# Kernel tuning notes

Hardware: AMD Instinct MI355X
Metric: run time of the kernel (lower is better)

## Reference

```python
import jax, jax.numpy as jnp
import numpy as np

N = 100000      # nodes
E = 3200000     # edges (before self-loops)
F_IN = 512      # input feature dim
HEADS = 8
DIM = 8         # per-head dim for hidden layers
HID = HEADS * DIM  # 64
CLS = 40        # num_classes
NEG_SLOPE = 0.2 # PyG GATConv default leaky relu slope


def setup_inputs() -> dict:
    key = jax.random.key(0)
    ks = jax.random.split(key, 14)
    def glorot(k, shape, fan_in):
        return jax.random.normal(k, shape, jnp.float32) * (1.0 / np.sqrt(fan_in))
    return {
        "x": jax.random.normal(ks[0], (N, F_IN), jnp.float32),
        "edge_index": jax.random.randint(ks[1], (2, E), 0, N, dtype=jnp.int32),
        # layer 1: in=F_IN, heads=8, dim=8, concat
        "W1": glorot(ks[2], (F_IN, HEADS * DIM), F_IN),
        "a_src1": glorot(ks[3], (HEADS, DIM), DIM),
        "a_dst1": glorot(ks[4], (HEADS, DIM), DIM),
        "b1": jnp.zeros((HEADS * DIM,), jnp.float32),
        # layer 2: in=64, heads=8, dim=8, concat
        "W2": glorot(ks[5], (HID, HEADS * DIM), HID),
        "a_src2": glorot(ks[6], (HEADS, DIM), DIM),
        "a_dst2": glorot(ks[7], (HEADS, DIM), DIM),
        "b2": jnp.zeros((HEADS * DIM,), jnp.float32),
        # layer 3: in=64, heads=1, dim=CLS, no concat (mean over heads == identity)
        "W3": glorot(ks[8], (HID, CLS), HID),
        "a_src3": glorot(ks[9], (1, CLS), CLS),
        "a_dst3": glorot(ks[10], (1, CLS), CLS),
        "b3": jnp.zeros((CLS,), jnp.float32),
    }


def gat_layer(h_in, W, att_src, att_dst, bias, src, dst, heads, dim, concat):
    # h_in: [N, F], W: [F, heads*dim], att_*: [heads, dim]
    n = h_in.shape[0]
    h = (h_in @ W).reshape(n, heads, dim)                    # [N, H, D]
    a_s = jnp.sum(h * att_src, axis=-1)                      # [N, H]
    a_d = jnp.sum(h * att_dst, axis=-1)                      # [N, H]
    e = jax.nn.leaky_relu(a_s[src] + a_d[dst], NEG_SLOPE)    # [E', H] edge logits
    # segment-softmax over incoming edges of each dst node (self-loops guarantee non-empty)
    m = jax.ops.segment_max(e, dst, num_segments=n)          # [N, H]
    p = jnp.exp(e - m[dst])
    s = jax.ops.segment_sum(p, dst, num_segments=n)          # [N, H]
    alpha = p / s[dst]                                       # [E', H]
    out = jax.ops.segment_sum(alpha[:, :, None] * h[src], dst, num_segments=n)  # [N, H, D]
    out = out.reshape(n, heads * dim) if concat else out.mean(axis=1)
    return out + bias


def reference(x, edge_index, W1, a_src1, a_dst1, b1, W2, a_src2, a_dst2, b2, W3, a_src3, a_dst3, b3):
    # PyG GATConv default add_self_loops=True
    loops = jnp.arange(N, dtype=edge_index.dtype)
    src = jnp.concatenate([edge_index[0], loops])
    dst = jnp.concatenate([edge_index[1], loops])
    h = gat_layer(x, W1, a_src1, a_dst1, b1, src, dst, HEADS, DIM, True)
    h = jax.nn.elu(h)  # dropout inactive in eval mode
    h = gat_layer(h, W2, a_src2, a_dst2, b2, src, dst, HEADS, DIM, True)
    h = jax.nn.elu(h)
    h = gat_layer(h, W3, a_src3, a_dst3, b3, src, dst, 1, CLS, False)
    return jax.nn.log_softmax(h, axis=1)
```

## Files before the change

kernel.cpp:

```cpp
#include <hip/hip_runtime.h>
#include <math.h>

#define NN 100000
#define EE 3200000
#define ET 3300000
#define FIN 512
#define HDIM 64
#define NCLS 40
#define OST3 64

#define NBUK 512
#define NPB 196
#define NBUK_USED 511
#define EPB 4096
#define EPT 16
#define CAP 8192
#define NCH 7

#define G1TILES 782
#define G1H 391
#define GBUK 806

typedef __attribute__((ext_vector_type(8))) short frag_ab;
typedef __attribute__((ext_vector_type(4))) float frag_cd;
typedef __attribute__((ext_vector_type(2))) float float2v;

#define CVTPK(dst, a, b) asm("v_cvt_pk_bf16_f32 %0, %1, %2" : "=v"(dst) : "v"(a), "v"(b))

__device__ inline unsigned short f2bf(float f){
  union { float f; unsigned int u; } x; x.f = f;
  unsigned int u = x.u;
  unsigned int r = u + 0x7FFF + ((u >> 16) & 1);
  return (unsigned short)(r >> 16);
}
__device__ inline unsigned char f2fp8(float v){
  int p = __builtin_amdgcn_cvt_pk_fp8_f32(v, v, 0, false);
  return (unsigned char)p;
}
__device__ inline float bflo(unsigned u){
  union { unsigned u; float f; } x; x.u = u << 16; return x.f;
}
__device__ inline float bfhi(unsigned u){
  union { unsigned u; float f; } x; x.u = u & 0xFFFF0000u; return x.f;
}
__device__ inline float bf2f(unsigned short u){
  union { unsigned int u; float f; } x; x.u = ((unsigned int)u) << 16;
  return x.f;
}
__device__ inline unsigned fkey(float f){
  union { float f; unsigned u; } x; x.f = f;
  return (x.u >> 31) ? ~x.u : (x.u | 0x80000000u);
}
__device__ inline float funkey(unsigned k){
  union { unsigned u; float f; } x;
  x.u = (k & 0x80000000u) ? (k ^ 0x80000000u) : ~k;
  return x.f;
}

__global__ void k_prep(const float* __restrict__ W1, const float* __restrict__ W2, const float* __restrict__ W3,
                       const float* __restrict__ as1, const float* __restrict__ ad1,
                       const float* __restrict__ as2, const float* __restrict__ ad2,
                       const float* __restrict__ as3, const float* __restrict__ ad3,
                       unsigned short* __restrict__ Wt1, unsigned short* __restrict__ Wt2,
                       unsigned short* __restrict__ Wt3, float* __restrict__ attv){
  int i = blockIdx.x*256 + threadIdx.x;
  if(i < 32768){
    int n = i >> 9, k = i & 511;
    Wt1[i] = f2bf(W1[k*HDIM + n]);
  } else if(i < 36864){
    int i2 = i - 32768; int n = i2 >> 6, k = i2 & 63;
    Wt2[i2] = f2bf(W2[k*HDIM + n]);
  } else if(i < 40960){
    int i3 = i - 36864; int n = i3 >> 6, k = i3 & 63;
    Wt3[i3] = (n < NCLS) ? f2bf(W3[k*NCLS + n]) : (unsigned short)0;
  } else if(i < 41312){
    int j = i - 40960;
    const float L2E = 1.4426950408889634f;
    float v;
    if(j < 64) v = as1[j]*L2E;
    else if(j < 128) v = ad1[j-64]*L2E;
    else if(j < 192) v = as2[j-128]*L2E;
    else if(j < 256) v = ad2[j-192]*L2E;
    else if(j < 304){ int q=j-256; v = (q<NCLS)? as3[q]*L2E : 0.f; }
    else { int q=j-304; v = (q<NCLS)? ad3[q]*L2E : 0.f; }
    attv[j] = v;
  }
}

template<int CT>
__device__ inline void att_epi8(const frag_cd (&acc)[2][CT], int rowbase, int fr, int kg,
                                const float* __restrict__ asv, const float* __restrict__ adv,
                                unsigned short* __restrict__ as_o, float* __restrict__ ad_o,
                                float (*gml)[8], int w, int M){
  float av[CT], dv[CT];
  #pragma unroll
  for(int j=0;j<CT;j++){ av[j]=asv[j*16+fr]; dv[j]=adv[j*16+fr]; }
  float mx[CT];
  #pragma unroll
  for(int j=0;j<CT;j++) mx[j] = -1e38f;
  #pragma unroll
  for(int i=0;i<2;i++){
    #pragma unroll
    for(int r=0;r<4;r++){
      int row = rowbase + i*16 + kg*4 + r;
      float ps[CT], pd[CT];
      #pragma unroll
      for(int j=0;j<CT;j++){ float v = acc[i][j][r]; ps[j]=v*av[j]; pd[j]=v*dv[j]; }
      #pragma unroll
      for(int mk=1; mk<8; mk<<=1){
        #pragma unroll
        for(int j=0;j<CT;j++){ ps[j]+=__shfl_xor(ps[j],mk); pd[j]+=__shfl_xor(pd[j],mk); }
      }
      if((fr&7)==0 && row < M){
        int half = fr>>3;
        uint2 s2;
        CVTPK(s2.x, ps[0], ps[1]);
        CVTPK(s2.y, ps[2], ps[3]);
        *(uint2*)&as_o[row*8 + half*4] = s2;
        float4 d4; d4.x=pd[0]; d4.y=pd[1]; d4.z=pd[2]; d4.w=pd[3];
        *(float4*)&ad_o[row*8 + half*4] = d4;
        #pragma unroll
        for(int j=0;j<CT;j++) mx[j] = fmaxf(mx[j], ps[j]);
      }
    }
  }
  #pragma unroll
  for(int j=0;j<CT;j++){
    mx[j] = fmaxf(mx[j], __shfl_xor(mx[j],16));
    mx[j] = fmaxf(mx[j], __shfl_xor(mx[j],32));
  }
  if(kg==0 && (fr&7)==0){
    int half = fr>>3;
    #pragma unroll
    for(int j=0;j<CT;j++) gml[w][half*4 + j] = mx[j];
  }
}

template<int CT>
__device__ inline void att_epi1(const frag_cd (&acc)[2][CT], int rowbase, int fr, int kg,
                                const float* __restrict__ asv, const float* __restrict__ adv,
                                float* __restrict__ as_o, float* __restrict__ ad_o,
                                float (*gml)[8], int w, int lane, int M){
  float av[CT], dv[CT];
  #pragma unroll
  for(int j=0;j<CT;j++){ av[j]=asv[j*16+fr]; dv[j]=adv[j*16+fr]; }
  float mx = -1e38f;
  #pragma unroll
  for(int i=0;i<2;i++){
    #pragma unroll
    for(int r=0;r<4;r++){
      int row = rowbase + i*16 + kg*4 + r;
      float ps=0.f, pd=0.f;
      #pragma unroll
      for(int j=0;j<CT;j++){ float v = acc[i][j][r]; ps += v*av[j]; pd += v*dv[j]; }
      #pragma unroll
      for(int mk=1; mk<16; mk<<=1){ ps+=__shfl_xor(ps,mk); pd+=__shfl_xor(pd,mk); }
      if(row < M){
        mx = fmaxf(mx, ps);
        if(fr==0){ as_o[row]=ps; ad_o[row]=pd; }
      }
    }
  }
  #pragma unroll
  for(int mk=1; mk<64; mk<<=1) mx = fmaxf(mx, __shfl_xor(mx, mk));
  if(lane==0) gml[w][0] = mx;
}

#define BM 128
#define BK 32
#define LSTR 40
template<int PHASE>
__global__ __launch_bounds__(256) void k_mix(const float* __restrict__ A, const unsigned short* __restrict__ Wt,
                                             const float* __restrict__ asv, const float* __restrict__ adv,
                                             unsigned char* __restrict__ Out8,
                                             unsigned short* __restrict__ as_o, float* __restrict__ ad_o,
                                             unsigned* __restrict__ gmax,
                                             const int* __restrict__ src, const int* __restrict__ dst,
                                             int* __restrict__ bcur, int* __restrict__ pbuf,
                                             int* __restrict__ rp, int* __restrict__ col){
  __shared__ __attribute__((aligned(16))) unsigned short Al[2][BM*LSTR];
  __shared__ __attribute__((aligned(16))) unsigned short Bl[2][64*LSTR];
  __shared__ float gml[4][8];
  int t = threadIdx.x;

  if(blockIdx.x >= G1H){
    int* shi = (int*)&Al[0][0];
    if(PHASE == 0){
      int bb = blockIdx.x - G1H;
      int* lcnt  = shi;
      int* lbase = shi + NBUK;
      for(int i=t;i<NBUK;i+=256) lcnt[i]=0;
      __syncthreads();
      int base = bb*EPB + t;
      int bk[EPT], rk[EPT], pk[EPT];
      #pragma unroll
      for(int j=0;j<EPT;j++){
        int e = base + j*256;
        bk[j] = -1;
        if(e < ET){
          int s, d;
          if(e < EE){ s = src[e]; d = dst[e]; } else { s = e - EE; d = s; }
          int b = d / NPB;
          bk[j] = b;
          pk[j] = s | ((d - b*NPB) << 17);
          rk[j] = atomicAdd(&lcnt[b], 1);
        }
      }
      __syncthreads();
      for(int i=t;i<NBUK;i+=256){
        int v = lcnt[i];
        lbase[i] = v ? atomicAdd(&bcur[i], v) : 0;
      }
      __syncthreads();
      #pragma unroll
      for(int j=0;j<EPT;j++){
        if(bk[j] >= 0){
          int pos = lbase[bk[j]] + rk[j];
          if(pos < CAP) pbuf[(size_t)bk[j]*CAP + pos] = pk[j];
        }
      }
    } else {
      int b = blockIdx.x - G1H;
      int* red = shi;
      int* cnt = shi + 256;
      int part = 0;
      for(int i=t; i<b; i+=256) part += bcur[i];
      red[t] = part;
      __syncthreads();
      for(int off=128; off; off>>=1){
        if(t < off) red[t] += red[t+off];
        __syncthreads();
      }
      int beg = red[0];
      int cntb = bcur[b];
      const int* pb = pbuf + (size_t)b*CAP;
      for(int i=t;i<NPB*NCH;i+=256) cnt[i]=0;
      __syncthreads();
      for(int i=t; i<cntb; i+=256){
        int v = pb[i];
        int dloc = v >> 17, s = v & 0x1FFFF;
        atomicAdd(&cnt[dloc*NCH + (s>>14)], 1);
      }
      __syncthreads();
      if(t < 64){
        int vals[22]; int sum = 0;
        #pragma unroll
        for(int j=0;j<22;j++){ int idx = t*22+j; int v = (idx<NPB*NCH)?cnt[idx]:0; vals[j]=v; sum+=v; }
        int incl = sum;
        #pragma unroll
        for(int off=1; off<64; off<<=1){
          int x = __shfl_up(incl, off);
          if(t >= off) incl += x;
        }
        int run = incl - sum;
        #pragma unroll
        for(int j=0;j<22;j++){
          int idx = t*22+j;
          if(idx < NPB*NCH){ int v = vals[j]; cnt[idx] = run; run += v; }
        }
      }
      __syncthreads();
      int node0 = b*NPB;
      int nloc = NN - node0; if(nloc > NPB) nloc = NPB;
      for(int i=t;i<nloc;i+=256) rp[node0 + i] = beg + cnt[i*NCH];
      if(b == 0 && t == 0) rp[NN] = ET;
      __syncthreads();
      for(int i=t; i<cntb; i+=256){
        int v = pb[i];
        int s = v & 0x1FFFF;
        int dloc = v >> 17;
        int pos = atomicAdd(&cnt[dloc*NCH + (s>>14)], 1);
        col[beg + pos] = s;
      }
    }
    return;
  }

  int w = t >> 6, l = t & 63;
  int row0 = (blockIdx.x + PHASE*G1H) * BM;
  int M = NN;

  int srow = t >> 1;
  int shalf = t & 1;
  int bn = t >> 2;
  int bseg = t & 3;
  int fr = l & 15, kg = l >> 4;

  frag_cd acc[2][4];
  #pragma unroll
  for(int i=0;i<2;i++)
    #pragma unroll
    for(int j=0;j<4;j++) acc[i][j] = (frag_cd){0.f,0.f,0.f,0.f};

  int rg = row0 + srow; if(rg >= M) rg = M-1;
  const float* aprow = &A[(size_t)rg*FIN + shalf*16];

  #define STAGE(buf, kc) do { \
    const float* ap = aprow + (kc); \
    float4 v0 = *(const float4*)(ap); \
    float4 v1 = *(const float4*)(ap+4); \
    float4 v2 = *(const float4*)(ap+8); \
    float4 v3 = *(const float4*)(ap+12); \
    uint4 pa, pb; \
    CVTPK(pa.x, v0.x, v0.y); CVTPK(pa.y, v0.z, v0.w); \
    CVTPK(pa.z, v1.x, v1.y); CVTPK(pa.w, v1.z, v1.w); \
    CVTPK(pb.x, v2.x, v2.y); CVTPK(pb.y, v2.z, v2.w); \
    CVTPK(pb.z, v3.x, v3.y); CVTPK(pb.w, v3.z, v3.w); \
    *(uint4*)&Al[buf][srow*LSTR + shalf*16] = pa; \
    *(uint4*)&Al[buf][srow*LSTR + shalf*16 + 8] = pb; \
    *(uint4*)&Bl[buf][bn*LSTR + bseg*8] = *(const uint4*)&Wt[bn*FIN + (kc) + bseg*8]; \
  } while(0)

  STAGE(0, 0);
  __syncthreads();

  #pragma unroll 1
  for(int step = 0; step < FIN/BK; ++step){
    int buf = step & 1;
    if(step + 1 < FIN/BK) STAGE(buf^1, (step+1)*BK);
    frag_ab af[2], bfr[4];
    #pragma unroll
    for(int i=0;i<2;i++) af[i] = *(const frag_ab*)&Al[buf][(w*32 + i*16 + fr)*LSTR + kg*8];
    #pragma unroll
    for(int j=0;j<4;j++) bfr[j] = *(const frag_ab*)&Bl[buf][(j*16 + fr)*LSTR + kg*8];
    #pragma unroll
    for(int i=0;i<2;i++)
      #pragma unroll
      for(int j=0;j<4;j++)
        acc[i][j] = __builtin_amdgcn_mfma_f32_16x16x32_bf16(af[i], bfr[j], acc[i][j], 0, 0, 0);
    __syncthreads();
  }

  #pragma unroll
  for(int i=0;i<2;i++){
    int crow = row0 + w*32 + i*16 + kg*4;
    #pragma unroll
    for(int j=0;j<4;j++){
      int ccol = j*16 + fr;
      #pragma unroll
      for(int r=0;r<4;r++){
        if(crow + r < M) Out8[(size_t)(crow+r)*HDIM + ccol] = f2fp8(acc[i][j][r]);
      }
    }
  }
  att_epi8(acc, row0 + w*32, fr, kg, asv, adv, as_o, ad_o, gml, w, M);
  __syncthreads();
  if(t < 8){
    float v = fmaxf(fmaxf(gml[0][t], gml[1][t]), fmaxf(gml[2][t], gml[3][t]));
    atomicMax(&gmax[t], fkey(v));
  }
  #undef STAGE
}

template<int K, int C, int OST, int HEADS>
__global__ __launch_bounds__(256) void k_gemmb(const unsigned short* __restrict__ A,
                                               const unsigned short* __restrict__ Wt,
                                               const float* __restrict__ asv, const float* __restrict__ adv,
                                               void* __restrict__ Outv,
                                               void* __restrict__ as_o, float* __restrict__ ad_o,
                                               unsigned* __restrict__ gmax, int M){
  constexpr int CT = (C + 15)/16;
  __shared__ __attribute__((aligned(16))) unsigned short Al[2][BM*LSTR];
  __shared__ __attribute__((aligned(16))) unsigned short Bl[2][64*LSTR];
  __shared__ float gml[4][8];
  int t = threadIdx.x;
  int w = t >> 6, l = t & 63;
  int row0 = blockIdx.x * BM;

  int srow = t >> 1;
  int shalf = t & 1;
  int bn = t >> 2;
  int bseg = t & 3;
  int fr = l & 15, kg = l >> 4;

  frag_cd acc[2][CT];
  #pragma unroll
  for(int i=0;i<2;i++)
    #pragma unroll
    for(int j=0;j<CT;j++) acc[i][j] = (frag_cd){0.f,0.f,0.f,0.f};

  int rg = row0 + srow; if(rg >= M) rg = M-1;
  const unsigned short* aprow = &A[(size_t)rg*K + shalf*16];

  #define STAGEB(buf, kc) do { \
    *(uint4*)&Al[buf][srow*LSTR + shalf*16]     = *(const uint4*)(aprow + (kc)); \
    *(uint4*)&Al[buf][srow*LSTR + shalf*16 + 8] = *(const uint4*)(aprow + (kc) + 8); \
    *(uint4*)&Bl[buf][bn*LSTR + bseg*8] = *(const uint4*)&Wt[bn*K + (kc) + bseg*8]; \
  } while(0)

  STAGEB(0, 0);
  __syncthreads();

  #pragma unroll 1
  for(int step = 0; step < K/BK; ++step){
    int buf = step & 1;
    if(step + 1 < K/BK) STAGEB(buf^1, (step+1)*BK);
    frag_ab af[2], bfr[CT];
    #pragma unroll
    for(int i=0;i<2;i++) af[i] = *(const frag_ab*)&Al[buf][(w*32 + i*16 + fr)*LSTR + kg*8];
    #pragma unroll
    for(int j=0;j<CT;j++) bfr[j] = *(const frag_ab*)&Bl[buf][(j*16 + fr)*LSTR + kg*8];
    #pragma unroll
    for(int i=0;i<2;i++)
      #pragma unroll
      for(int j=0;j<CT;j++)
        acc[i][j] = __builtin_amdgcn_mfma_f32_16x16x32_bf16(af[i], bfr[j], acc[i][j], 0, 0, 0);
    __syncthreads();
  }

  #pragma unroll
  for(int i=0;i<2;i++){
    int crow = row0 + w*32 + i*16 + kg*4;
    #pragma unroll
    for(int j=0;j<CT;j++){
      int ccol = j*16 + fr;
      if(ccol >= C) continue;
      #pragma unroll
      for(int r=0;r<4;r++){
        if(crow + r < M){
          if(HEADS == 8) ((unsigned char*)Outv)[(size_t)(crow+r)*HDIM + ccol] = f2fp8(acc[i][j][r]);
          else           ((unsigned short*)Outv)[(size_t)(crow+r)*OST + ccol] = f2bf(acc[i][j][r]);
        }
      }
    }
  }
  if(HEADS == 8){
    att_epi8(acc, row0 + w*32, fr, kg, asv, adv, (unsigned short*)as_o, ad_o, gml, w, M);
    __syncthreads();
    if(t < 8){
      float v = fmaxf(fmaxf(gml[0][t], gml[1][t]), fmaxf(gml[2][t], gml[3][t]));
      atomicMax(&gmax[t], fkey(v));
    }
  } else {
    att_epi1(acc, row0 + w*32, fr, kg, asv, adv, (float*)as_o, ad_o, gml, w, l, M);
    __syncthreads();
    if(t == 0){
      float v = fmaxf(fmaxf(gml[0][0], gml[1][0]), fmaxf(gml[2][0], gml[3][0]));
      atomicMax(&gmax[0], fkey(v));
    }
  }
  #undef STAGEB
}

template<bool DO_ELU>
__global__ __launch_bounds__(256) void k_agg8(const unsigned char* __restrict__ h8, const int* __restrict__ rp,
                      const int* __restrict__ col,
                      const unsigned short* __restrict__ asb, const float* __restrict__ ad_,
                      const unsigned* __restrict__ gmax,
                      const float* __restrict__ bias, unsigned short* __restrict__ out){
  int gid = blockIdx.x*256 + threadIdx.x;
  int node = gid >> 6, lane = gid & 63;
  if(node >= NN) return;
  int el = lane >> 3;
  int fl = lane & 7;
  int px = ((fl&1)<<2) | (fl>>1);
  int beg = rp[node], end = rp[node+1];
  int deg = end - beg;
  float adn = ad_[node*8 + px];
  float M = funkey(gmax[px]) + adn;
  M = fmaxf(M, 0.2f*M);
  float s = 0.f;
  float a[8] = {0.f,0.f,0.f,0.f,0.f,0.f,0.f,0.f};

  for(int base = 0; base < deg; base += 64){
    int cnt = deg - base; if(cnt > 64) cnt = 64;
    int idx = 0;
    if(lane < cnt) idx = col[beg + base + lane];
    int jf = cnt & ~7;
    int j = 0;
    for(; j < jf; j += 8){
      int sn = __shfl(idx, j + el);
      float ea = bf2f(asb[sn*8 + px]);
      uint2 h = *(const uint2*)&h8[(size_t)sn*HDIM + fl*8];
      float e = ea + adn; e = fmaxf(e, 0.2f*e);
      float p = exp2f(e - M);
      s += p;
      float2v q0 = __builtin_amdgcn_cvt_pk_f32_fp8(h.x, false);
      float2v q1 = __builtin_amdgcn_cvt_pk_f32_fp8(h.x, true);
      float2v q2 = __builtin_amdgcn_cvt_pk_f32_fp8(h.y, false);
      float2v q3 = __builtin_amdgcn_cvt_pk_f32_fp8(h.y, true);
      a[0] = fmaf(p, q0.x, a[0]); a[1] = fmaf(p, q0.y, a[1]);
      a[2] = fmaf(p, q1.x, a[2]); a[3] = fmaf(p, q1.y, a[3]);
      a[4] = fmaf(p, q2.x, a[4]); a[5] = fmaf(p, q2.y, a[5]);
      a[6] = fmaf(p, q3.x, a[6]); a[7] = fmaf(p, q3.y, a[7]);
    }
    if(j < cnt){
      int sn = __shfl(idx, j + el);
      float ea = bf2f(asb[sn*8 + px]);
      uint2 h = *(const uint2*)&h8[(size_t)sn*HDIM + fl*8];
      float e = ea + adn; e = fmaxf(e, 0.2f*e);
      float p = (j + el < cnt) ? exp2f(e - M) : 0.f;
      s += p;
      float2v q0 = __builtin_amdgcn_cvt_pk_f32_fp8(h.x, false);
      float2v q1 = __builtin_amdgcn_cvt_pk_f32_fp8(h.x, true);
      float2v q2 = __builtin_amdgcn_cvt_pk_f32_fp8(h.y, false);
      float2v q3 = __builtin_amdgcn_cvt_pk_f32_fp8(h.y, true);
      a[0] = fmaf(p, q0.x, a[0]); a[1] = fmaf(p, q0.y, a[1]);
      a[2] = fmaf(p, q1.x, a[2]); a[3] = fmaf(p, q1.y, a[3]);
      a[4] = fmaf(p, q2.x, a[4]); a[5] = fmaf(p, q2.y, a[5]);
      a[6] = fmaf(p, q3.x, a[6]); a[7] = fmaf(p, q3.y, a[7]);
    }
  }

  #pragma unroll
  for(int wd=8; wd<=32; wd<<=1){
    s += __shfl_xor(s, wd);
    #pragma unroll
    for(int i=0;i<8;i++) a[i] += __shfl_xor(a[i], wd);
  }

  if(el == 0){
    float inv = 1.f/s;
    float4 b0 = *(const float4*)&bias[fl*8];
    float4 b1 = *(const float4*)&bias[fl*8 + 4];
    float o[8];
    o[0]=a[0]*inv+b0.x; o[1]=a[1]*inv+b0.y; o[2]=a[2]*inv+b0.z; o[3]=a[3]*inv+b0.w;
    o[4]=a[4]*inv+b1.x; o[5]=a[5]*inv+b1.y; o[6]=a[6]*inv+b1.z; o[7]=a[7]*inv+b1.w;
    if(DO_ELU){
      #pragma unroll
      for(int i=0;i<8;i++) o[i] = (o[i] > 0.f) ? o[i] : expm1f(o[i]);
    }
    uint4 pk;
    CVTPK(pk.x, o[0], o[1]); CVTPK(pk.y, o[2], o[3]);
    CVTPK(pk.z, o[4], o[5]); CVTPK(pk.w, o[6], o[7]);
    *(uint4*)&out[(size_t)node*HDIM + fl*8] = pk;
  }
}

__global__ __launch_bounds__(256) void k_agg1(const unsigned short* __restrict__ hbf, const int* __restrict__ rp,
                      const int* __restrict__ col,
                      const float* __restrict__ as_, const float* __restrict__ ad_,
                      const unsigned* __restrict__ gmax,
                      const float* __restrict__ bias, float* __restrict__ out){
  int gid = blockIdx.x*256 + threadIdx.x;
  int node = gid >> 6, lane = gid & 63;
  if(node >= NN) return;
  int el = lane >> 3;
  int fl = lane & 7;
  bool act = fl < 5;
  int f0 = act ? fl*8 : 0;
  int beg = rp[node], end = rp[node+1];
  int deg = end - beg;
  float adn = ad_[node];
  float M = funkey(gmax[0]) + adn;
  M = fmaxf(M, 0.2f*M);
  float s = 0.f;
  float a[8] = {0.f,0.f,0.f,0.f,0.f,0.f,0.f,0.f};

  for(int base = 0; base < deg; base += 64){
    int cnt = deg - base; if(cnt > 64) cnt = 64;
    int idx = 0;
    if(lane < cnt) idx = col[beg + base + lane];
    for(int j = 0; j < cnt; j += 8){
      int sn = __shfl(idx, j + el);
      float ea = as_[sn];
      uint4 h = *(const uint4*)&hbf[(size_t)sn*OST3 + f0];
      float e = ea + adn; e = fmaxf(e, 0.2f*e);
      float p = (j + el < cnt) ? exp2f(e - M) : 0.f;
      s += p;
      a[0] = fmaf(p, bflo(h.x), a[0]); a[1] = fmaf(p, bfhi(h.x), a[1]);
      a[2] = fmaf(p, bflo(h.y), a[2]); a[3] = fmaf(p, bfhi(h.y), a[3]);
      a[4] = fmaf(p, bflo(h.z), a[4]); a[5] = fmaf(p, bfhi(h.z), a[5]);
      a[6] = fmaf(p, bflo(h.w), a[6]); a[7] = fmaf(p, bfhi(h.w), a[7]);
    }
  }

  #pragma unroll
  for(int wd=8; wd<=32; wd<<=1){
    s += __shfl_xor(s, wd);
    #pragma unroll
    for(int i=0;i<8;i++) a[i] += __shfl_xor(a[i], wd);
  }

  float inv = 1.f/s;
  float o[8];
  #pragma unroll
  for(int i=0;i<8;i++) o[i] = a[i]*inv + (act ? bias[f0+i] : 0.f);

  float vmax = act ? fmaxf(fmaxf(fmaxf(o[0],o[1]),fmaxf(o[2],o[3])),
                           fmaxf(fmaxf(o[4],o[5]),fmaxf(o[6],o[7]))) : -INFINITY;
  #pragma unroll
  for(int wd=1; wd<8; wd<<=1) vmax = fmaxf(vmax, __shfl_xor(vmax, wd));
  float ex = 0.f;
  if(act){
    #pragma unroll
    for(int i=0;i<8;i++) ex += expf(o[i] - vmax);
  }
  #pragma unroll
  for(int wd=1; wd<8; wd<<=1) ex += __shfl_xor(ex, wd);
  float lg = logf(ex);
  if(el == 0 && act){
    float4 r0, r1;
    r0.x=o[0]-vmax-lg; r0.y=o[1]-vmax-lg; r0.z=o[2]-vmax-lg; r0.w=o[3]-vmax-lg;
    r1.x=o[4]-vmax-lg; r1.y=o[5]-vmax-lg; r1.z=o[6]-vmax-lg; r1.w=o[7]-vmax-lg;
    *(float4*)&out[(size_t)node*NCLS + f0]     = r0;
    *(float4*)&out[(size_t)node*NCLS + f0 + 4] = r1;
  }
}

static inline size_t alignup(size_t x){ return (x + 255) & ~(size_t)255; }

extern "C" void kernel_launch(void* const* d_in, const int* in_sizes, int n_in,
                              void* d_out, int out_size, void* d_ws, size_t ws_size,
                              hipStream_t stream){
  const float* x      = (const float*)d_in[0];
  const int*   ei     = (const int*)d_in[1];
  const float* W1     = (const float*)d_in[2];
  const float* asrc1  = (const float*)d_in[3];
  const float* adst1  = (const float*)d_in[4];
  const float* b1     = (const float*)d_in[5];
  const float* W2     = (const float*)d_in[6];
  const float* asrc2  = (const float*)d_in[7];
  const float* adst2  = (const float*)d_in[8];
  const float* b2     = (const float*)d_in[9];
  const float* W3     = (const float*)d_in[10];
  const float* asrc3  = (const float*)d_in[11];
  const float* adst3  = (const float*)d_in[12];
  const float* b3     = (const float*)d_in[13];
  const int* src = ei;
  const int* dst = ei + EE;

  char* w = (char*)d_ws;
  int* rp     = (int*)w;              w += alignup((size_t)(NN+1)*4);
  int* bcur   = (int*)w;              w += alignup((size_t)NBUK*4);
  unsigned* gmax = (unsigned*)w;      w += alignup(32*4);
  unsigned short* Wt1 = (unsigned short*)w; w += alignup((size_t)64*FIN*2);
  unsigned short* Wt2 = (unsigned short*)w; w += alignup((size_t)64*HDIM*2);
  unsigned short* Wt3 = (unsigned short*)w; w += alignup((size_t)64*HDIM*2);
  float* attv = (float*)w;            w += alignup((size_t)352*4);
  int* col    = (int*)w;              w += alignup((size_t)ET*4);
  int* pbuf   = (int*)w;              w += alignup((size_t)NBUK*CAP*4);
  unsigned char* hA8 = (unsigned char*)w; w += alignup((size_t)NN*HDIM + 256);
  unsigned short* hBb = (unsigned short*)w; w += alignup((size_t)NN*HDIM*2 + 256);
  unsigned short* hCb = (unsigned short*)w; w += alignup((size_t)NN*OST3*2 + 256);
  unsigned short* asb = (unsigned short*)w; w += alignup((size_t)NN*8*2 + 256);
  float* as3  = (float*)w;            w += alignup((size_t)NN*4);
  float* adA  = (float*)w;            w += alignup((size_t)NN*8*4);

  dim3 blk(256);
  int gWav  = (NN*64 + 255)/256;
  int gG1   = (NN + BM - 1)/BM;

  hipMemsetAsync(bcur, 0, 2048 + 128, stream);
  k_prep<<<(41312 + 255)/256, blk, 0, stream>>>(W1, W2, W3, asrc1, adst1, asrc2, adst2, asrc3, adst3,
                                                Wt1, Wt2, Wt3, attv);
  k_mix<0><<<G1H + GBUK, blk, 0, stream>>>(x, Wt1, attv + 0, attv + 64, hA8, asb, adA, gmax + 0,
                                           src, dst, bcur, pbuf, rp, col);
  k_mix<1><<<G1H + NBUK_USED, blk, 0, stream>>>(x, Wt1, attv + 0, attv + 64, hA8, asb, adA, gmax + 0,
                                                src, dst, bcur, pbuf, rp, col);

  k_agg8<true><<<gWav, blk, 0, stream>>>(hA8, rp, col, asb, adA, gmax + 0, b1, hBb);

  k_gemmb<HDIM, HDIM, HDIM, 8><<<gG1, blk, 0, stream>>>(hBb, Wt2, attv + 128, attv + 192, hA8, asb, adA, gmax + 8, NN);
  k_agg8<true><<<gWav, blk, 0, stream>>>(hA8, rp, col, asb, adA, gmax + 8, b2, hBb);

  k_gemmb<HDIM, NCLS, OST3, 1><<<gG1, blk, 0, stream>>>(hBb, Wt3, attv + 256, attv + 304, hCb, as3, adA, gmax + 16, NN);
  k_agg1<<<gWav, blk, 0, stream>>>(hCb, rp, col, as3, adA, gmax + 16, b3, (float*)d_out);
}
```

Baseline: 386.9 us.

## Process two heads per lane in fp8 aggregation with 16 edges in flight

The attention-score epilogue now writes per-head scores in a plain head order instead of the old permuted half layout. This lets each aggregation lane load two adjacent heads' bf16 source scores with one 32-bit load. The aggregation kernel switches from 8 lanes × 8 features to 4 lanes × 16 features per edge, so each wave handles 16 edges per step with 16-byte fp8 feature loads. This means fewer iterations, wider loads and fewer per-edge score loads. In exchange, the per-lane accumulator state and the cross-lane reduction grow, which raises register pressure, and the epilogue now does scalar stores instead of packed vector stores.

```diff
diff --git a/kernel.cpp b/kernel.cpp
--- a/kernel.cpp
+++ b/kernel.cpp
@@ -113,14 +113,12 @@
       }
       if((fr&7)==0 && row < M){
         int half = fr>>3;
-        uint2 s2;
-        CVTPK(s2.x, ps[0], ps[1]);
-        CVTPK(s2.y, ps[2], ps[3]);
-        *(uint2*)&as_o[row*8 + half*4] = s2;
-        float4 d4; d4.x=pd[0]; d4.y=pd[1]; d4.z=pd[2]; d4.w=pd[3];
-        *(float4*)&ad_o[row*8 + half*4] = d4;
         #pragma unroll
-        for(int j=0;j<CT;j++) mx[j] = fmaxf(mx[j], ps[j]);
+        for(int j=0;j<CT;j++){
+          as_o[row*8 + 2*j + half] = f2bf(ps[j]);
+          ad_o[row*8 + 2*j + half] = pd[j];
+          mx[j] = fmaxf(mx[j], ps[j]);
+        }
       }
     }
   }
@@ -132,7 +130,7 @@
   if(kg==0 && (fr&7)==0){
     int half = fr>>3;
     #pragma unroll
-    for(int j=0;j<CT;j++) gml[w][half*4 + j] = mx[j];
+    for(int j=0;j<CT;j++) gml[w][2*j + half] = mx[j];
   }
 }
 
@@ -451,79 +449,95 @@
   int gid = blockIdx.x*256 + threadIdx.x;
   int node = gid >> 6, lane = gid & 63;
   if(node >= NN) return;
-  int el = lane >> 3;
-  int fl = lane & 7;
-  int px = ((fl&1)<<2) | (fl>>1);
+  int el = lane >> 2;
+  int fl = lane & 3;
+  int f0 = fl*16;
+  int h2 = fl*2;
+  float2 adn = *(const float2*)&ad_[node*8 + h2];
+  float M0 = funkey(gmax[h2])   + adn.x; M0 = fmaxf(M0, 0.2f*M0);
+  float M1 = funkey(gmax[h2+1]) + adn.y; M1 = fmaxf(M1, 0.2f*M1);
   int beg = rp[node], end = rp[node+1];
   int deg = end - beg;
-  float adn = ad_[node*8 + px];
-  float M = funkey(gmax[px]) + adn;
-  M = fmaxf(M, 0.2f*M);
-  float s = 0.f;
-  float a[8] = {0.f,0.f,0.f,0.f,0.f,0.f,0.f,0.f};
+  float s0 = 0.f, s1 = 0.f;
+  float a[16] = {0.f,0.f,0.f,0.f,0.f,0.f,0.f,0.f,0.f,0.f,0.f,0.f,0.f,0.f,0.f,0.f};
 
   for(int base = 0; base < deg; base += 64){
     int cnt = deg - base; if(cnt > 64) cnt = 64;
     int idx = 0;
     if(lane < cnt) idx = col[beg + base + lane];
-    int jf = cnt & ~7;
+    int jf = cnt & ~15;
     int j = 0;
-    for(; j < jf; j += 8){
+    for(; j < jf; j += 16){
       int sn = __shfl(idx, j + el);
-      float ea = bf2f(asb[sn*8 + px]);
-      uint2 h = *(const uint2*)&h8[(size_t)sn*HDIM + fl*8];
-      float e = ea + adn; e = fmaxf(e, 0.2f*e);
-      float p = exp2f(e - M);
-      s += p;
-      float2v q0 = __builtin_amdgcn_cvt_pk_f32_fp8(h.x, false);
-      float2v q1 = __builtin_amdgcn_cvt_pk_f32_fp8(h.x, true);
-      float2v q2 = __builtin_amdgcn_cvt_pk_f32_fp8(h.y, false);
-      float2v q3 = __builtin_amdgcn_cvt_pk_f32_fp8(h.y, true);
-      a[0] = fmaf(p, q0.x, a[0]); a[1] = fmaf(p, q0.y, a[1]);
-      a[2] = fmaf(p, q1.x, a[2]); a[3] = fmaf(p, q1.y, a[3]);
-      a[4] = fmaf(p, q2.x, a[4]); a[5] = fmaf(p, q2.y, a[5]);
-      a[6] = fmaf(p, q3.x, a[6]); a[7] = fmaf(p, q3.y, a[7]);
+      unsigned av = *(const unsigned*)&asb[sn*8 + h2];
+      uint4 h = *(const uint4*)&h8[(size_t)sn*HDIM + f0];
+      float e0 = bflo(av) + adn.x; e0 = fmaxf(e0, 0.2f*e0);
+      float e1 = bfhi(av) + adn.y; e1 = fmaxf(e1, 0.2f*e1);
+      float p0 = exp2f(e0 - M0);
+      float p1 = exp2f(e1 - M1);
+      s0 += p0; s1 += p1;
+      float2v q;
+      q = __builtin_amdgcn_cvt_pk_f32_fp8(h.x,false); a[0]=fmaf(p0,q.x,a[0]);  a[1]=fmaf(p0,q.y,a[1]);
+      q = __builtin_amdgcn_cvt_pk_f32_fp8(h.x,true);  a[2]=fmaf(p0,q.x,a[2]);  a[3]=fmaf(p0,q.y,a[3]);
+      q = __builtin_amdgcn_cvt_pk_f32_fp8(h.y,false); a[4]=fmaf(p0,q.x,a[4]);  a[5]=fmaf(p0,q.y,a[5]);
+      q = __builtin_amdgcn_cvt_pk_f32_fp8(h.y,true);  a[6]=fmaf(p0,q.x,a[6]);  a[7]=fmaf(p0,q.y,a[7]);
+      q = __builtin_amdgcn_cvt_pk_f32_fp8(h.z,false); a[8]=fmaf(p1,q.x,a[8]);  a[9]=fmaf(p1,q.y,a[9]);
+      q = __builtin_amdgcn_cvt_pk_f32_fp8(h.z,true);  a[10]=fmaf(p1,q.x,a[10]); a[11]=fmaf(p1,q.y,a[11]);
+      q = __builtin_amdgcn_cvt_pk_f32_fp8(h.w,false); a[12]=fmaf(p1,q.x,a[12]); a[13]=fmaf(p1,q.y,a[13]);
+      q = __builtin_amdgcn_cvt_pk_f32_fp8(h.w,true);  a[14]=fmaf(p1,q.x,a[14]); a[15]=fmaf(p1,q.y,a[15]);
     }
     if(j < cnt){
       int sn = __shfl(idx, j + el);
-      float ea = bf2f(asb[sn*8 + px]);
-      uint2 h = *(const uint2*)&h8[(size_t)sn*HDIM + fl*8];
-      float e = ea + adn; e = fmaxf(e, 0.2f*e);
-      float p = (j + el < cnt) ? exp2f(e - M) : 0.f;
-      s += p;
-      float2v q0 = __builtin_amdgcn_cvt_pk_f32_fp8(h.x, false);
-      float2v q1 = __builtin_amdgcn_cvt_pk_f32_fp8(h.x, true);
-      float2v q2 = __builtin_amdgcn_cvt_pk_f32_fp8(h.y, false);
-      float2v q3 = __builtin_amdgcn_cvt_pk_f32_fp8(h.y, true);
-      a[0] = fmaf(p, q0.x, a[0]); a[1] = fmaf(p, q0.y, a[1]);
-      a[2] = fmaf(p, q1.x, a[2]); a[3] = fmaf(p, q1.y, a[3]);
-      a[4] = fmaf(p, q2.x, a[4]); a[5] = fmaf(p, q2.y, a[5]);
-      a[6] = fmaf(p, q3.x, a[6]); a[7] = fmaf(p, q3.y, a[7]);
-    }
-  }
-
-  #pragma unroll
-  for(int wd=8; wd<=32; wd<<=1){
-    s += __shfl_xor(s, wd);
-    #pragma unroll
-    for(int i=0;i<8;i++) a[i] += __shfl_xor(a[i], wd);
+      bool v = (j + el) < cnt;
+      unsigned av = *(const unsigned*)&asb[sn*8 + h2];
+      uint4 h = *(const uint4*)&h8[(size_t)sn*HDIM + f0];
+      float e0 = bflo(av) + adn.x; e0 = fmaxf(e0, 0.2f*e0);
+      float e1 = bfhi(av) + adn.y; e1 = fmaxf(e1, 0.2f*e1);
+      float p0 = v ? exp2f(e0 - M0) : 0.f;
+      float p1 = v ? exp2f(e1 - M1) : 0.f;
+      s0 += p0; s1 += p1;
+      float2v q;
+      q = __builtin_amdgcn_cvt_pk_f32_fp8(h.x,false); a[0]=fmaf(p0,q.x,a[0]);  a[1]=fmaf(p0,q.y,a[1]);
+      q = __builtin_amdgcn_cvt_pk_f32_fp8(h.x,true);  a[2]=fmaf(p0,q.x,a[2]);  a[3]=fmaf(p0,q.y,a[3]);
+      q = __builtin_amdgcn_cvt_pk_f32_fp8(h.y,false); a[4]=fmaf(p0,q.x,a[4]);  a[5]=fmaf(p0,q.y,a[5]);
+      q = __builtin_amdgcn_cvt_pk_f32_fp8(h.y,true);  a[6]=fmaf(p0,q.x,a[6]);  a[7]=fmaf(p0,q.y,a[7]);
+      q = __builtin_amdgcn_cvt_pk_f32_fp8(h.z,false); a[8]=fmaf(p1,q.x,a[8]);  a[9]=fmaf(p1,q.y,a[9]);
+      q = __builtin_amdgcn_cvt_pk_f32_fp8(h.z,true);  a[10]=fmaf(p1,q.x,a[10]); a[11]=fmaf(p1,q.y,a[11]);
+      q = __builtin_amdgcn_cvt_pk_f32_fp8(h.w,false); a[12]=fmaf(p1,q.x,a[12]); a[13]=fmaf(p1,q.y,a[13]);
+      q = __builtin_amdgcn_cvt_pk_f32_fp8(h.w,true);  a[14]=fmaf(p1,q.x,a[14]); a[15]=fmaf(p1,q.y,a[15]);
+    }
+  }
+
+  #pragma unroll
+  for(int wd=4; wd<=32; wd<<=1){
+    s0 += __shfl_xor(s0, wd);
+    s1 += __shfl_xor(s1, wd);
+    #pragma unroll
+    for(int i=0;i<16;i++) a[i] += __shfl_xor(a[i], wd);
   }
 
   if(el == 0){
-    float inv = 1.f/s;
-    float4 b0 = *(const float4*)&bias[fl*8];
-    float4 b1 = *(const float4*)&bias[fl*8 + 4];
-    float o[8];
-    o[0]=a[0]*inv+b0.x; o[1]=a[1]*inv+b0.y; o[2]=a[2]*inv+b0.z; o[3]=a[3]*inv+b0.w;
-    o[4]=a[4]*inv+b1.x; o[5]=a[5]*inv+b1.y; o[6]=a[6]*inv+b1.z; o[7]=a[7]*inv+b1.w;
+    float i0 = 1.f/s0, i1 = 1.f/s1;
+    float4 b0 = *(const float4*)&bias[f0];
+    float4 b1 = *(const float4*)&bias[f0+4];
+    float4 b2 = *(const float4*)&bias[f0+8];
+    float4 b3 = *(const float4*)&bias[f0+12];
+    float o[16];
+    o[0]=a[0]*i0+b0.x;  o[1]=a[1]*i0+b0.y;  o[2]=a[2]*i0+b0.z;  o[3]=a[3]*i0+b0.w;
+    o[4]=a[4]*i0+b1.x;  o[5]=a[5]*i0+b1.y;  o[6]=a[6]*i0+b1.z;  o[7]=a[7]*i0+b1.w;
+    o[8]=a[8]*i1+b2.x;  o[9]=a[9]*i1+b2.y;  o[10]=a[10]*i1+b2.z; o[11]=a[11]*i1+b2.w;
+    o[12]=a[12]*i1+b3.x; o[13]=a[13]*i1+b3.y; o[14]=a[14]*i1+b3.z; o[15]=a[15]*i1+b3.w;
     if(DO_ELU){
       #pragma unroll
-      for(int i=0;i<8;i++) o[i] = (o[i] > 0.f) ? o[i] : expm1f(o[i]);
-    }
-    uint4 pk;
-    CVTPK(pk.x, o[0], o[1]); CVTPK(pk.y, o[2], o[3]);
-    CVTPK(pk.z, o[4], o[5]); CVTPK(pk.w, o[6], o[7]);
-    *(uint4*)&out[(size_t)node*HDIM + fl*8] = pk;
+      for(int i=0;i<16;i++) o[i] = (o[i] > 0.f) ? o[i] : expm1f(o[i]);
+    }
+    uint4 pk0, pk1;
+    CVTPK(pk0.x, o[0], o[1]);  CVTPK(pk0.y, o[2], o[3]);
+    CVTPK(pk0.z, o[4], o[5]);  CVTPK(pk0.w, o[6], o[7]);
+    CVTPK(pk1.x, o[8], o[9]);  CVTPK(pk1.y, o[10], o[11]);
+    CVTPK(pk1.z, o[12], o[13]); CVTPK(pk1.w, o[14], o[15]);
+    *(uint4*)&out[(size_t)node*HDIM + f0]     = pk0;
+    *(uint4*)&out[(size_t)node*HDIM + f0 + 8] = pk1;
   }
 }
 
```

Result: slower. 417.8 us (+8.0%).
